# Kernel tuning notes

Hardware: AMD Instinct MI355X
Metric: run time of the kernel (lower is better)

## Reference

```python
import jax, jax.numpy as jnp
from jax import lax
import numpy as np

B, S_DEC, S_ENC = 32, 128, 128
V, E, H = 32000, 200, 128


def setup_inputs() -> dict:
    key = jax.random.key(0)
    ks = jax.random.split(key, 10)
    emb = jax.random.normal(ks[0], (V, E), dtype=jnp.float32)
    emb = emb.at[0].set(0.0)  # padding_idx row (char2id[' '] -> 0)
    return {
        "sequence": jax.random.randint(ks[1], (B, S_DEC), 0, V),
        "hs": jax.random.normal(ks[2], (B, S_ENC, H), dtype=jnp.float32),
        "h": jax.random.normal(ks[3], (1, B, H), dtype=jnp.float32),
        "emb": emb,
        "w_ih": jax.random.normal(ks[4], (3 * H, E), dtype=jnp.float32) * 0.05,
        "w_hh": jax.random.normal(ks[5], (3 * H, H), dtype=jnp.float32) * 0.05,
        "b_ih": jax.random.normal(ks[6], (3 * H,), dtype=jnp.float32) * 0.05,
        "b_hh": jax.random.normal(ks[7], (3 * H,), dtype=jnp.float32) * 0.05,
        "w_out": jax.random.normal(ks[8], (V, 2 * H), dtype=jnp.float32) * 0.05,
        "b_out": jax.random.normal(ks[9], (V,), dtype=jnp.float32) * 0.05,
    }


def _gru(x_gates, h0, w_hh, b_hh):
    # x_gates: [B, S, 3H] precomputed input projections; torch gate order r,z,n
    def step(hprev, xg):
        hg = hprev @ w_hh.T + b_hh
        xr, xz, xn = jnp.split(xg, 3, axis=-1)
        hr, hz, hn = jnp.split(hg, 3, axis=-1)
        r = jax.nn.sigmoid(xr + hr)
        z = jax.nn.sigmoid(xz + hz)
        n = jnp.tanh(xn + r * hn)
        hnew = (1.0 - z) * n + z * hprev
        return hnew, hnew

    hT, outs = lax.scan(step, h0, jnp.swapaxes(x_gates, 0, 1))  # scan over time
    return jnp.swapaxes(outs, 0, 1), hT  # [B,S,H], [B,H]


def reference(sequence, hs, h, emb, w_ih, w_hh, b_ih, b_hh, w_out, b_out):
    # Embedding lookup (padding row already zero)
    x = emb[sequence]  # [B, S_dec, E]
    x_gates = jnp.einsum("bse,ge->bsg", x, w_ih) + b_ih  # [B, S_dec, 3H]
    output, hT = _gru(x_gates, h[0], w_hh, b_hh)  # [B, S_dec, H]
    state = hT[None]  # [1, B, H]
    # s = bmm(hs, output^T): [B, S_enc, S_dec]; softmax over encoder axis (dim=1)
    s = jnp.einsum("beh,bdh->bed", hs, output)
    attention_weight = jax.nn.softmax(s, axis=1)
    # context: replaces the per-timestep python loop with one contraction
    c = jnp.einsum("bed,beh->bdh", attention_weight, hs)  # [B, S_dec, H]
    cat = jnp.concatenate([output, c], axis=-1)  # [B, S_dec, 2H]
    logits = jnp.einsum("bdh,vh->bdv", cat, w_out) + b_out  # [B, S_dec, V]
    return logits, state, attention_weight
```

## Files before the change

kernel.cpp:

```cpp
#include <hip/hip_runtime.h>
#include <hip/hip_bf16.h>

#define B_    32
#define SDEC  128
#define SENC  128
#define V_    32000
#define E_    200
#define H_    128
#define G3    384

typedef __attribute__((ext_vector_type(8))) short bf16x8;
typedef __attribute__((ext_vector_type(4))) float f32x4;

#define GLOBAL_AS __attribute__((address_space(1)))
#define LDS_AS    __attribute__((address_space(3)))

__device__ __forceinline__ float fast_sigmoid(float x) {
  return 1.f / (1.f + __expf(-x));
}
__device__ __forceinline__ float fast_tanh(float x) {
  float e2 = __expf(2.f * x);
  return 1.f - 2.f / (e2 + 1.f);
}

__global__ __launch_bounds__(384) void k_embed_proj(
    const int* __restrict__ seq, const float* __restrict__ emb,
    const float* __restrict__ w_ih, const float* __restrict__ b_ih,
    float* __restrict__ xg) {
  __shared__ __align__(16) float xs[16][E_];
  __shared__ int sidx[16];
  const int r0 = blockIdx.x * 16;
  if (threadIdx.x < 16) sidx[threadIdx.x] = seq[r0 + threadIdx.x];
  __syncthreads();
  for (int i = threadIdx.x; i < 800; i += 384) {
    int r = i / 50, c = i - r * 50;
    *(float4*)&xs[r][c * 4] =
        *(const float4*)(emb + (size_t)sidx[r] * E_ + c * 4);
  }
  __syncthreads();
  const int g = threadIdx.x;
  float acc[16];
#pragma unroll
  for (int r = 0; r < 16; r++) acc[r] = 0.f;
  const float* wg = w_ih + (size_t)g * E_;
  for (int k = 0; k < E_; k += 4) {
    float4 wv = *(const float4*)(wg + k);
#pragma unroll
    for (int r = 0; r < 16; r++) {
      float4 xv = *(const float4*)&xs[r][k];
      acc[r] += wv.x * xv.x + wv.y * xv.y + wv.z * xv.z + wv.w * xv.w;
    }
  }
  const float bb = b_ih[g];
#pragma unroll
  for (int r = 0; r < 16; r++) xg[(size_t)(r0 + r) * G3 + g] = acc[r] + bb;
}

__global__ __launch_bounds__(512) void k_gru_cvt(
    const float* __restrict__ xg, const float* __restrict__ h0,
    const float* __restrict__ w_hh, const float* __restrict__ b_hh,
    float* __restrict__ cat, __hip_bfloat16* __restrict__ cat_bf,
    float* __restrict__ state_out,
    const float* __restrict__ w_out, __hip_bfloat16* __restrict__ wout_bf) {
  if (blockIdx.x >= 32) {
    int idx = ((blockIdx.x - 32) * 512 + threadIdx.x) * 8;
    float4 a = *(const float4*)(w_out + idx);
    float4 c = *(const float4*)(w_out + idx + 4);
    union { __hip_bfloat16 h[8]; uint4 v; } p;
    p.h[0] = __float2bfloat16(a.x); p.h[1] = __float2bfloat16(a.y);
    p.h[2] = __float2bfloat16(a.z); p.h[3] = __float2bfloat16(a.w);
    p.h[4] = __float2bfloat16(c.x); p.h[5] = __float2bfloat16(c.y);
    p.h[6] = __float2bfloat16(c.z); p.h[7] = __float2bfloat16(c.w);
    *(uint4*)(wout_bf + idx) = p.v;
    return;
  }

  const int b = blockIdx.x;
  const int t = threadIdx.x;
  const int hh = t & 127;
  const int q = t >> 7;

  float wr_[32], wz_[32], wn_[32];
#pragma unroll
  for (int j4 = 0; j4 < 8; j4++) {
    *(float4*)&wr_[j4 * 4] =
        *(const float4*)(w_hh + (size_t)hh * H_ + q * 32 + j4 * 4);
    *(float4*)&wz_[j4 * 4] =
        *(const float4*)(w_hh + (size_t)(128 + hh) * H_ + q * 32 + j4 * 4);
    *(float4*)&wn_[j4 * 4] =
        *(const float4*)(w_hh + (size_t)(256 + hh) * H_ + q * 32 + j4 * 4);
  }

  __shared__ __align__(16) float hprev[H_];
  __shared__ float part[3][4][H_];
  float br = 0.f, bz = 0.f, bn = 0.f;
  float cxr = 0.f, cxz = 0.f, cxn = 0.f;
  const float* xgb = xg + (size_t)b * SDEC * G3;
  if (t < H_) {
    hprev[t] = h0[b * H_ + t];
    br = b_hh[hh]; bz = b_hh[128 + hh]; bn = b_hh[256 + hh];
    cxr = xgb[hh]; cxz = xgb[128 + hh]; cxn = xgb[256 + hh];
  }
  float* catb = cat + (size_t)b * SDEC * 256;
  __hip_bfloat16* catbfb = cat_bf + (size_t)b * SDEC * 256;
  __syncthreads();

  for (int s = 0; s < SDEC; s++) {
    float nxr = 0.f, nxz = 0.f, nxn = 0.f;
    if (t < H_ && s + 1 < SDEC) {
      const float* xp = xgb + (size_t)(s + 1) * G3;
      nxr = xp[hh]; nxz = xp[128 + hh]; nxn = xp[256 + hh];
    }
    float sr = 0.f, sz = 0.f, sn = 0.f;
#pragma unroll
    for (int j4 = 0; j4 < 8; j4++) {
      float4 hv = *(const float4*)&hprev[q * 32 + j4 * 4];
      sr += wr_[j4 * 4 + 0] * hv.x + wr_[j4 * 4 + 1] * hv.y +
            wr_[j4 * 4 + 2] * hv.z + wr_[j4 * 4 + 3] * hv.w;
      sz += wz_[j4 * 4 + 0] * hv.x + wz_[j4 * 4 + 1] * hv.y +
            wz_[j4 * 4 + 2] * hv.z + wz_[j4 * 4 + 3] * hv.w;
      sn += wn_[j4 * 4 + 0] * hv.x + wn_[j4 * 4 + 1] * hv.y +
            wn_[j4 * 4 + 2] * hv.z + wn_[j4 * 4 + 3] * hv.w;
    }
    part[0][q][hh] = sr;
    part[1][q][hh] = sz;
    part[2][q][hh] = sn;
    __syncthreads();
    if (t < H_) {
      float hr = part[0][0][hh] + part[0][1][hh] + part[0][2][hh] + part[0][3][hh] + br;
      float hz = part[1][0][hh] + part[1][1][hh] + part[1][2][hh] + part[1][3][hh] + bz;
      float hn = part[2][0][hh] + part[2][1][hh] + part[2][2][hh] + part[2][3][hh] + bn;
      float r = fast_sigmoid(cxr + hr);
      float z = fast_sigmoid(cxz + hz);
      float n = fast_tanh(cxn + r * hn);
      float hnew = (1.f - z) * n + z * hprev[hh];
      hprev[hh] = hnew;
      catb[(size_t)s * 256 + hh] = hnew;
      catbfb[(size_t)s * 256 + hh] = __float2bfloat16(hnew);
    }
    __syncthreads();
    cxr = nxr; cxz = nxz; cxn = nxn;
  }
  if (t < H_) state_out[b * H_ + t] = hprev[t];
}

__global__ __launch_bounds__(256) void k_attn(
    const float* __restrict__ hs, const float* __restrict__ cat,
    float* __restrict__ attw_out, __hip_bfloat16* __restrict__ cat_bf) {
  __shared__ float hsb[SENC][H_ + 1];
  __shared__ float ctb[64][H_ + 1];
  __shared__ float sbuf[SENC][64 + 1];
  const int b = blockIdx.x >> 1;
  const int d0 = (blockIdx.x & 1) * 64;
  const int t = threadIdx.x;
  const float* hsbase = hs + (size_t)b * SENC * H_;

  for (int i = t; i < 4096; i += 256) {
    int r = i >> 5, c = (i & 31) * 4;
    float4 v = *(const float4*)(hsbase + r * H_ + c);
    hsb[r][c] = v.x; hsb[r][c + 1] = v.y; hsb[r][c + 2] = v.z; hsb[r][c + 3] = v.w;
  }
  for (int i = t; i < 2048; i += 256) {
    int r = i >> 5, c = (i & 31) * 4;
    float4 v = *(const float4*)(cat + (size_t)(b * SDEC + d0 + r) * 256 + c);
    ctb[r][c] = v.x; ctb[r][c + 1] = v.y; ctb[r][c + 2] = v.z; ctb[r][c + 3] = v.w;
  }
  __syncthreads();

  {
    const int te = t >> 4, td = t & 15;
    float acc[8][4];
#pragma unroll
    for (int i = 0; i < 8; i++)
#pragma unroll
      for (int j = 0; j < 4; j++) acc[i][j] = 0.f;
#pragma unroll 2
    for (int k = 0; k < H_; k++) {
      float av[8], bv[4];
#pragma unroll
      for (int i = 0; i < 8; i++) av[i] = hsb[te * 8 + i][k];
#pragma unroll
      for (int j = 0; j < 4; j++) bv[j] = ctb[td * 4 + j][k];
#pragma unroll
      for (int i = 0; i < 8; i++)
#pragma unroll
        for (int j = 0; j < 4; j++) acc[i][j] += av[i] * bv[j];
    }
#pragma unroll
    for (int i = 0; i < 8; i++)
#pragma unroll
      for (int j = 0; j < 4; j++) sbuf[te * 8 + i][td * 4 + j] = acc[i][j];
  }
  __syncthreads();

  if (t < 64) {
    const int d = t;
    float m = -1e30f;
    for (int e = 0; e < SENC; e++) m = fmaxf(m, sbuf[e][d]);
    float sum = 0.f;
    for (int e = 0; e < SENC; e++) {
      float p = __expf(sbuf[e][d] - m);
      sbuf[e][d] = p;
      sum += p;
    }
    float inv = 1.f / sum;
    for (int e = 0; e < SENC; e++) {
      float p = sbuf[e][d] * inv;
      sbuf[e][d] = p;
      attw_out[(size_t)b * SENC * SDEC + (size_t)e * SDEC + d0 + d] = p;
    }
  }
  __syncthreads();

  {
    const int td = t >> 4, th = t & 15;
    float acc[4][8];
#pragma unroll
    for (int i = 0; i < 4; i++)
#pragma unroll
      for (int j = 0; j < 8; j++) acc[i][j] = 0.f;
#pragma unroll 2
    for (int e = 0; e < SENC; e++) {
      float pv[4], hv[8];
#pragma unroll
      for (int i = 0; i < 4; i++) pv[i] = sbuf[e][td * 4 + i];
#pragma unroll
      for (int j = 0; j < 8; j++) hv[j] = hsb[e][th + 16 * j];
#pragma unroll
      for (int i = 0; i < 4; i++)
#pragma unroll
        for (int j = 0; j < 8; j++) acc[i][j] += pv[i] * hv[j];
    }
#pragma unroll
    for (int i = 0; i < 4; i++)
#pragma unroll
      for (int j = 0; j < 8; j++)
        cat_bf[(size_t)(b * SDEC + d0 + td * 4 + i) * 256 + 128 + th + 16 * j] =
            __float2bfloat16(acc[i][j]);
  }
}

__global__ __launch_bounds__(512) void k_gemm_mfma(
    const __hip_bfloat16* __restrict__ A, const __hip_bfloat16* __restrict__ Bw,
    const float* __restrict__ b_out, float* __restrict__ C) {
  constexpr int K = 256, N = V_, Kt = 32;
  alignas(16) __shared__ char smem[73728];
  __hip_bfloat16 (*As)[4096] = (__hip_bfloat16(*)[4096])smem;
  __hip_bfloat16 (*Bs)[8192] = (__hip_bfloat16(*)[8192])(smem + 24576);
  float* tr = (float*)smem;

  const int tid = threadIdx.x;
  const int w = tid >> 6, l = tid & 63;
  const int wr = w >> 2, wc = w & 3;
  const int lr = l & 15, lk = l >> 4;
  const int lq = l >> 2, lc = l & 3;

  const int bid = blockIdx.x;
  const int wgid = (bid & 7) * 500 + (bid >> 3);
  const int mt = wgid & 31;
  const int nt = wgid >> 5;
  const int m0 = mt * 128, n0 = nt * 256;

  f32x4 acc[4][4];
#pragma unroll
  for (int m = 0; m < 4; m++)
#pragma unroll
    for (int n = 0; n < 4; n++) acc[m][n] = (f32x4){0.f, 0.f, 0.f, 0.f};

#define STAGE(buf, kk)                                                            \
  do {                                                                            \
    const __hip_bfloat16* gA = A + (size_t)(m0 + w * 16 + lq) * K + (kk) + lc * 8;\
    const __hip_bfloat16* gB0 = Bw + (size_t)(n0 + w * 32 + lq) * K + (kk) + lc * 8;\
    const __hip_bfloat16* gB1 = gB0 + (size_t)16 * K;                             \
    __builtin_amdgcn_global_load_lds((const GLOBAL_AS void*)gA,                   \
        (LDS_AS void*)(&As[buf][w * 512]), 16, 0, 0);                             \
    __builtin_amdgcn_global_load_lds((const GLOBAL_AS void*)gB0,                  \
        (LDS_AS void*)(&Bs[buf][w * 1024]), 16, 0, 0);                            \
    __builtin_amdgcn_global_load_lds((const GLOBAL_AS void*)gB1,                  \
        (LDS_AS void*)(&Bs[buf][w * 1024 + 512]), 16, 0, 0);                      \
  } while (0)

  STAGE(0, 0);
  STAGE(1, Kt);

#pragma unroll
  for (int t = 0; t < 8; ++t) {
    if (t < 7) asm volatile("s_waitcnt vmcnt(3)" ::: "memory");
    else       asm volatile("s_waitcnt vmcnt(0)" ::: "memory");
    __builtin_amdgcn_s_barrier();
    asm volatile("" ::: "memory");

    const int c = t % 3;
    bf16x8 af[4], bfr[4];
#pragma unroll
    for (int m = 0; m < 4; m++)
      af[m] = *(const bf16x8*)(const void*)(&As[c][(wr * 64 + m * 16 + lr) * Kt + lk * 8]);
#pragma unroll
    for (int n = 0; n < 4; n++)
      bfr[n] = *(const bf16x8*)(const void*)(&Bs[c][(wc * 64 + n * 16 + lr) * Kt + lk * 8]);

    if (t < 6) STAGE((t + 2) % 3, (t + 2) * Kt);

#pragma unroll
    for (int m = 0; m < 4; m++)
#pragma unroll
      for (int n = 0; n < 4; n++)
        acc[m][n] = __builtin_amdgcn_mfma_f32_16x16x32_bf16(bfr[n], af[m], acc[m][n], 0, 0, 0);
  }
#undef STAGE

  __syncthreads();
#pragma unroll
  for (int h = 0; h < 2; ++h) {
    if (wr == h) {
#pragma unroll
      for (int m = 0; m < 4; m++) {
#pragma unroll
        for (int n = 0; n < 4; n++) {
          const int row = m * 16 + lr;
          const int col = wc * 64 + n * 16 + lk * 4;
          const float4 bo = *(const float4*)(b_out + n0 + col);
          f32x4 v;
          v[0] = acc[m][n][0] + bo.x;
          v[1] = acc[m][n][1] + bo.y;
          v[2] = acc[m][n][2] + bo.z;
          v[3] = acc[m][n][3] + bo.w;
          *(f32x4*)&tr[row * 260 + col] = v;
        }
      }
    }
    __syncthreads();
#pragma unroll
    for (int i = 0; i < 8; ++i) {
      const int c2 = i * 512 + tid;
      const int row = c2 >> 6;
      const int off = (c2 & 63) * 4;
      f32x4 v = *(const f32x4*)&tr[row * 260 + off];
      __builtin_nontemporal_store(
          v, (f32x4*)(C + (size_t)(m0 + h * 64 + row) * N + n0 + off));
    }
    __syncthreads();
  }
}

extern "C" void kernel_launch(void* const* d_in, const int* in_sizes, int n_in,
                              void* d_out, int out_size, void* d_ws, size_t ws_size,
                              hipStream_t stream) {
  const int* seq = (const int*)d_in[0];
  const float* hs = (const float*)d_in[1];
  const float* h0 = (const float*)d_in[2];
  const float* emb = (const float*)d_in[3];
  const float* w_ih = (const float*)d_in[4];
  const float* w_hh = (const float*)d_in[5];
  const float* b_ih = (const float*)d_in[6];
  const float* b_hh = (const float*)d_in[7];
  const float* w_out = (const float*)d_in[8];
  const float* b_out = (const float*)d_in[9];

  float* out = (float*)d_out;
  float* logits = out;
  float* state = out + 131072000;
  float* attw = out + 131072000 + 4096;

  char* ws = (char*)d_ws;
  float* xg = (float*)ws;
  float* cat = (float*)(ws + 6291456);
  __hip_bfloat16* cat_bf = (__hip_bfloat16*)(ws + 10485760);
  __hip_bfloat16* wout_bf = (__hip_bfloat16*)(ws + 12582912);

  k_embed_proj<<<256, 384, 0, stream>>>(seq, emb, w_ih, b_ih, xg);
  k_gru_cvt<<<2032, 512, 0, stream>>>(xg, h0, w_hh, b_hh, cat, cat_bf, state,
                                      w_out, wout_bf);
  k_attn<<<64, 256, 0, stream>>>(hs, cat, attw, cat_bf);
  k_gemm_mfma<<<4000, 512, 0, stream>>>(cat_bf, wout_bf, b_out, logits);
}
```

Measured before the change: 287.4 us.

## Rework GRU reduction via shuffles, swizzle attention LDS, halve embed-proj threads

The GRU recurrence now gives four adjacent lanes to each hidden unit and reduces their partial dot products with wave shuffles instead of an LDS partial buffer. It double-buffers the hidden state, which removes one barrier per timestep. The attention kernel drops padded LDS arrays in favour of XOR-swizzled float4 layouts, vectorizes the score, softmax and context loops, and writes the bf16 context with packed 16-byte stores. The embedding projection uses 192 threads that each compute two gate rows. The swizzle index arithmetic adds complexity and risks bank conflicts or indexing errors if the permutations are wrong.

```diff
diff --git a/kernel.cpp b/kernel.cpp
--- a/kernel.cpp
+++ b/kernel.cpp
@@ -23,37 +23,44 @@
   return 1.f - 2.f / (e2 + 1.f);
 }
 
-__global__ __launch_bounds__(384) void k_embed_proj(
+__global__ __launch_bounds__(192) void k_embed_proj(
     const int* __restrict__ seq, const float* __restrict__ emb,
     const float* __restrict__ w_ih, const float* __restrict__ b_ih,
     float* __restrict__ xg) {
   __shared__ __align__(16) float xs[16][E_];
   __shared__ int sidx[16];
   const int r0 = blockIdx.x * 16;
-  if (threadIdx.x < 16) sidx[threadIdx.x] = seq[r0 + threadIdx.x];
-  __syncthreads();
-  for (int i = threadIdx.x; i < 800; i += 384) {
+  const int t = threadIdx.x;
+  if (t < 16) sidx[t] = seq[r0 + t];
+  __syncthreads();
+  for (int i = t; i < 800; i += 192) {
     int r = i / 50, c = i - r * 50;
     *(float4*)&xs[r][c * 4] =
         *(const float4*)(emb + (size_t)sidx[r] * E_ + c * 4);
   }
   __syncthreads();
-  const int g = threadIdx.x;
-  float acc[16];
-#pragma unroll
-  for (int r = 0; r < 16; r++) acc[r] = 0.f;
-  const float* wg = w_ih + (size_t)g * E_;
+  const int g0 = t, g1 = t + 192;
+  float a0[16], a1[16];
+#pragma unroll
+  for (int r = 0; r < 16; r++) { a0[r] = 0.f; a1[r] = 0.f; }
+  const float* w0 = w_ih + (size_t)g0 * E_;
+  const float* w1 = w_ih + (size_t)g1 * E_;
   for (int k = 0; k < E_; k += 4) {
-    float4 wv = *(const float4*)(wg + k);
+    float4 wv0 = *(const float4*)(w0 + k);
+    float4 wv1 = *(const float4*)(w1 + k);
 #pragma unroll
     for (int r = 0; r < 16; r++) {
       float4 xv = *(const float4*)&xs[r][k];
-      acc[r] += wv.x * xv.x + wv.y * xv.y + wv.z * xv.z + wv.w * xv.w;
-    }
-  }
-  const float bb = b_ih[g];
-#pragma unroll
-  for (int r = 0; r < 16; r++) xg[(size_t)(r0 + r) * G3 + g] = acc[r] + bb;
+      a0[r] += wv0.x * xv.x + wv0.y * xv.y + wv0.z * xv.z + wv0.w * xv.w;
+      a1[r] += wv1.x * xv.x + wv1.y * xv.y + wv1.z * xv.z + wv1.w * xv.w;
+    }
+  }
+  const float b0 = b_ih[g0], b1 = b_ih[g1];
+#pragma unroll
+  for (int r = 0; r < 16; r++) {
+    xg[(size_t)(r0 + r) * G3 + g0] = a0[r] + b0;
+    xg[(size_t)(r0 + r) * G3 + g1] = a1[r] + b1;
+  }
 }
 
 __global__ __launch_bounds__(512) void k_gru_cvt(
@@ -77,166 +84,195 @@
 
   const int b = blockIdx.x;
   const int t = threadIdx.x;
-  const int hh = t & 127;
-  const int q = t >> 7;
+  const int hh = t >> 2;
+  const int sub = t & 3;
 
   float wr_[32], wz_[32], wn_[32];
 #pragma unroll
-  for (int j4 = 0; j4 < 8; j4++) {
-    *(float4*)&wr_[j4 * 4] =
-        *(const float4*)(w_hh + (size_t)hh * H_ + q * 32 + j4 * 4);
-    *(float4*)&wz_[j4 * 4] =
-        *(const float4*)(w_hh + (size_t)(128 + hh) * H_ + q * 32 + j4 * 4);
-    *(float4*)&wn_[j4 * 4] =
-        *(const float4*)(w_hh + (size_t)(256 + hh) * H_ + q * 32 + j4 * 4);
-  }
-
-  __shared__ __align__(16) float hprev[H_];
-  __shared__ float part[3][4][H_];
-  float br = 0.f, bz = 0.f, bn = 0.f;
-  float cxr = 0.f, cxz = 0.f, cxn = 0.f;
+  for (int m = 0; m < 8; m++) {
+    int c = (m + sub * 2) & 7;
+    int kb = sub * 32 + c * 4;
+    *(float4*)&wr_[m * 4] = *(const float4*)(w_hh + (size_t)hh * H_ + kb);
+    *(float4*)&wz_[m * 4] = *(const float4*)(w_hh + (size_t)(128 + hh) * H_ + kb);
+    *(float4*)&wn_[m * 4] = *(const float4*)(w_hh + (size_t)(256 + hh) * H_ + kb);
+  }
+
+  __shared__ __align__(16) float hp[2][H_];
   const float* xgb = xg + (size_t)b * SDEC * G3;
-  if (t < H_) {
-    hprev[t] = h0[b * H_ + t];
-    br = b_hh[hh]; bz = b_hh[128 + hh]; bn = b_hh[256 + hh];
-    cxr = xgb[hh]; cxz = xgb[128 + hh]; cxn = xgb[256 + hh];
-  }
+  const float br = b_hh[hh], bz = b_hh[128 + hh], bn = b_hh[256 + hh];
+  float cxr = xgb[hh], cxz = xgb[128 + hh], cxn = xgb[256 + hh];
+  if (t < H_) hp[0][t] = h0[b * H_ + t];
   float* catb = cat + (size_t)b * SDEC * 256;
   __hip_bfloat16* catbfb = cat_bf + (size_t)b * SDEC * 256;
   __syncthreads();
 
+  int cur = 0;
   for (int s = 0; s < SDEC; s++) {
     float nxr = 0.f, nxz = 0.f, nxn = 0.f;
-    if (t < H_ && s + 1 < SDEC) {
+    if (s + 1 < SDEC) {
       const float* xp = xgb + (size_t)(s + 1) * G3;
       nxr = xp[hh]; nxz = xp[128 + hh]; nxn = xp[256 + hh];
     }
     float sr = 0.f, sz = 0.f, sn = 0.f;
 #pragma unroll
-    for (int j4 = 0; j4 < 8; j4++) {
-      float4 hv = *(const float4*)&hprev[q * 32 + j4 * 4];
-      sr += wr_[j4 * 4 + 0] * hv.x + wr_[j4 * 4 + 1] * hv.y +
-            wr_[j4 * 4 + 2] * hv.z + wr_[j4 * 4 + 3] * hv.w;
-      sz += wz_[j4 * 4 + 0] * hv.x + wz_[j4 * 4 + 1] * hv.y +
-            wz_[j4 * 4 + 2] * hv.z + wz_[j4 * 4 + 3] * hv.w;
-      sn += wn_[j4 * 4 + 0] * hv.x + wn_[j4 * 4 + 1] * hv.y +
-            wn_[j4 * 4 + 2] * hv.z + wn_[j4 * 4 + 3] * hv.w;
-    }
-    part[0][q][hh] = sr;
-    part[1][q][hh] = sz;
-    part[2][q][hh] = sn;
-    __syncthreads();
-    if (t < H_) {
-      float hr = part[0][0][hh] + part[0][1][hh] + part[0][2][hh] + part[0][3][hh] + br;
-      float hz = part[1][0][hh] + part[1][1][hh] + part[1][2][hh] + part[1][3][hh] + bz;
-      float hn = part[2][0][hh] + part[2][1][hh] + part[2][2][hh] + part[2][3][hh] + bn;
-      float r = fast_sigmoid(cxr + hr);
-      float z = fast_sigmoid(cxz + hz);
-      float n = fast_tanh(cxn + r * hn);
-      float hnew = (1.f - z) * n + z * hprev[hh];
-      hprev[hh] = hnew;
+    for (int m = 0; m < 8; m++) {
+      int c = (m + sub * 2) & 7;
+      float4 hv = *(const float4*)&hp[cur][sub * 32 + c * 4];
+      sr += wr_[m * 4 + 0] * hv.x + wr_[m * 4 + 1] * hv.y +
+            wr_[m * 4 + 2] * hv.z + wr_[m * 4 + 3] * hv.w;
+      sz += wz_[m * 4 + 0] * hv.x + wz_[m * 4 + 1] * hv.y +
+            wz_[m * 4 + 2] * hv.z + wz_[m * 4 + 3] * hv.w;
+      sn += wn_[m * 4 + 0] * hv.x + wn_[m * 4 + 1] * hv.y +
+            wn_[m * 4 + 2] * hv.z + wn_[m * 4 + 3] * hv.w;
+    }
+    sr += __shfl_xor(sr, 1); sr += __shfl_xor(sr, 2);
+    sz += __shfl_xor(sz, 1); sz += __shfl_xor(sz, 2);
+    sn += __shfl_xor(sn, 1); sn += __shfl_xor(sn, 2);
+
+    float hold = hp[cur][hh];
+    float r = fast_sigmoid(cxr + sr + br);
+    float z = fast_sigmoid(cxz + sz + bz);
+    float n = fast_tanh(cxn + r * (sn + bn));
+    float hnew = (1.f - z) * n + z * hold;
+    if (sub == 0) {
+      hp[cur ^ 1][hh] = hnew;
       catb[(size_t)s * 256 + hh] = hnew;
       catbfb[(size_t)s * 256 + hh] = __float2bfloat16(hnew);
     }
     __syncthreads();
+    cur ^= 1;
     cxr = nxr; cxz = nxz; cxn = nxn;
   }
-  if (t < H_) state_out[b * H_ + t] = hprev[t];
+  if (t < H_) state_out[b * H_ + t] = hp[cur][t];
 }
 
 __global__ __launch_bounds__(256) void k_attn(
     const float* __restrict__ hs, const float* __restrict__ cat,
     float* __restrict__ attw_out, __hip_bfloat16* __restrict__ cat_bf) {
-  __shared__ float hsb[SENC][H_ + 1];
-  __shared__ float ctb[64][H_ + 1];
-  __shared__ float sbuf[SENC][64 + 1];
+  __shared__ __align__(16) float hsb[SENC][H_];
+  __shared__ __align__(16) float ctb[64][H_];
+  __shared__ __align__(16) float sbuf[64][SENC];
   const int b = blockIdx.x >> 1;
   const int d0 = (blockIdx.x & 1) * 64;
   const int t = threadIdx.x;
   const float* hsbase = hs + (size_t)b * SENC * H_;
 
   for (int i = t; i < 4096; i += 256) {
-    int r = i >> 5, c = (i & 31) * 4;
-    float4 v = *(const float4*)(hsbase + r * H_ + c);
-    hsb[r][c] = v.x; hsb[r][c + 1] = v.y; hsb[r][c + 2] = v.z; hsb[r][c + 3] = v.w;
+    int r = i >> 5, c4 = i & 31;
+    int pc = c4 ^ ((r >> 3) & 3);
+    *(f32x4*)&hsb[r][pc * 4] = *(const f32x4*)(hsbase + r * H_ + c4 * 4);
   }
   for (int i = t; i < 2048; i += 256) {
-    int r = i >> 5, c = (i & 31) * 4;
-    float4 v = *(const float4*)(cat + (size_t)(b * SDEC + d0 + r) * 256 + c);
-    ctb[r][c] = v.x; ctb[r][c + 1] = v.y; ctb[r][c + 2] = v.z; ctb[r][c + 3] = v.w;
+    int r = i >> 5, c4 = i & 31;
+    int pc = c4 ^ ((r >> 2) & 7);
+    *(f32x4*)&ctb[r][pc * 4] =
+        *(const f32x4*)(cat + (size_t)(b * SDEC + d0 + r) * 256 + c4 * 4);
   }
   __syncthreads();
 
   {
     const int te = t >> 4, td = t & 15;
-    float acc[8][4];
-#pragma unroll
-    for (int i = 0; i < 8; i++)
-#pragma unroll
-      for (int j = 0; j < 4; j++) acc[i][j] = 0.f;
-#pragma unroll 2
-    for (int k = 0; k < H_; k++) {
-      float av[8], bv[4];
-#pragma unroll
-      for (int i = 0; i < 8; i++) av[i] = hsb[te * 8 + i][k];
-#pragma unroll
-      for (int j = 0; j < 4; j++) bv[j] = ctb[td * 4 + j][k];
+    const int sa = te & 3, sb2 = td & 7;
+    float acc[8][4] = {};
+    for (int k4 = 0; k4 < 32; k4++) {
+      const int pa = (k4 ^ sa) * 4, pb = (k4 ^ sb2) * 4;
+      f32x4 av[8], bv[4];
+#pragma unroll
+      for (int i = 0; i < 8; i++) av[i] = *(const f32x4*)&hsb[te * 8 + i][pa];
+#pragma unroll
+      for (int j = 0; j < 4; j++) bv[j] = *(const f32x4*)&ctb[td * 4 + j][pb];
 #pragma unroll
       for (int i = 0; i < 8; i++)
 #pragma unroll
-        for (int j = 0; j < 4; j++) acc[i][j] += av[i] * bv[j];
-    }
-#pragma unroll
-    for (int i = 0; i < 8; i++)
-#pragma unroll
-      for (int j = 0; j < 4; j++) sbuf[te * 8 + i][td * 4 + j] = acc[i][j];
-  }
-  __syncthreads();
-
-  if (t < 64) {
-    const int d = t;
-    float m = -1e30f;
-    for (int e = 0; e < SENC; e++) m = fmaxf(m, sbuf[e][d]);
+        for (int j = 0; j < 4; j++)
+          acc[i][j] += av[i][0] * bv[j][0] + av[i][1] * bv[j][1] +
+                       av[i][2] * bv[j][2] + av[i][3] * bv[j][3];
+    }
+    const int swd = td & 7;
+#pragma unroll
+    for (int j = 0; j < 4; j++) {
+      int drow = td * 4 + j;
+      f32x4 v0 = {acc[0][j], acc[1][j], acc[2][j], acc[3][j]};
+      f32x4 v1 = {acc[4][j], acc[5][j], acc[6][j], acc[7][j]};
+      *(f32x4*)&sbuf[drow][((te * 2) ^ swd) * 4] = v0;
+      *(f32x4*)&sbuf[drow][((te * 2 + 1) ^ swd) * 4] = v1;
+    }
+  }
+  __syncthreads();
+
+  {
+    const int d = t >> 2, p = t & 3;
+    const int swz = (d >> 2) & 7;
+    f32x4 vals[8];
+    float mx = -1e30f;
+#pragma unroll
+    for (int mm = 0; mm < 8; mm++) {
+      int pc = p * 8 + mm;
+      f32x4 v = *(const f32x4*)&sbuf[d][pc * 4];
+      vals[mm] = v;
+      mx = fmaxf(mx, fmaxf(fmaxf(v[0], v[1]), fmaxf(v[2], v[3])));
+    }
+    mx = fmaxf(mx, __shfl_xor(mx, 1));
+    mx = fmaxf(mx, __shfl_xor(mx, 2));
     float sum = 0.f;
-    for (int e = 0; e < SENC; e++) {
-      float p = __expf(sbuf[e][d] - m);
-      sbuf[e][d] = p;
-      sum += p;
-    }
-    float inv = 1.f / sum;
-    for (int e = 0; e < SENC; e++) {
-      float p = sbuf[e][d] * inv;
-      sbuf[e][d] = p;
-      attw_out[(size_t)b * SENC * SDEC + (size_t)e * SDEC + d0 + d] = p;
+#pragma unroll
+    for (int mm = 0; mm < 8; mm++) {
+      f32x4 v = vals[mm];
+      v[0] = __expf(v[0] - mx); v[1] = __expf(v[1] - mx);
+      v[2] = __expf(v[2] - mx); v[3] = __expf(v[3] - mx);
+      vals[mm] = v;
+      sum += v[0] + v[1] + v[2] + v[3];
+    }
+    sum += __shfl_xor(sum, 1); sum += __shfl_xor(sum, 2);
+    const float inv = 1.f / sum;
+    float* aw = attw_out + (size_t)b * SENC * SDEC + d0 + d;
+#pragma unroll
+    for (int mm = 0; mm < 8; mm++) {
+      int pc = p * 8 + mm;
+      f32x4 v = vals[mm];
+      v[0] *= inv; v[1] *= inv; v[2] *= inv; v[3] *= inv;
+      *(f32x4*)&sbuf[d][pc * 4] = v;
+      int c4 = pc ^ swz;
+#pragma unroll
+      for (int u = 0; u < 4; u++)
+        aw[(size_t)(c4 * 4 + u) * SDEC] = v[u];
     }
   }
   __syncthreads();
 
   {
     const int td = t >> 4, th = t & 15;
-    float acc[4][8];
-#pragma unroll
-    for (int i = 0; i < 4; i++)
-#pragma unroll
-      for (int j = 0; j < 8; j++) acc[i][j] = 0.f;
-#pragma unroll 2
-    for (int e = 0; e < SENC; e++) {
-      float pv[4], hv[8];
-#pragma unroll
-      for (int i = 0; i < 4; i++) pv[i] = sbuf[e][td * 4 + i];
-#pragma unroll
-      for (int j = 0; j < 8; j++) hv[j] = hsb[e][th + 16 * j];
-#pragma unroll
-      for (int i = 0; i < 4; i++)
-#pragma unroll
-        for (int j = 0; j < 8; j++) acc[i][j] += pv[i] * hv[j];
-    }
-#pragma unroll
-    for (int i = 0; i < 4; i++)
-#pragma unroll
-      for (int j = 0; j < 8; j++)
-        cat_bf[(size_t)(b * SDEC + d0 + td * 4 + i) * 256 + 128 + th + 16 * j] =
-            __float2bfloat16(acc[i][j]);
+    const int swd = td & 7;
+    float acc[4][8] = {};
+    for (int e4 = 0; e4 < 32; e4++) {
+      const int pp = (e4 ^ swd) * 4;
+      f32x4 pv[4];
+#pragma unroll
+      for (int i = 0; i < 4; i++) pv[i] = *(const f32x4*)&sbuf[td * 4 + i][pp];
+#pragma unroll
+      for (int j = 0; j < 4; j++) {
+        int e = e4 * 4 + j;
+        int sw = (e >> 3) & 3;
+        f32x4 h0v = *(const f32x4*)&hsb[e][((th * 2) ^ sw) * 4];
+        f32x4 h1v = *(const f32x4*)&hsb[e][((th * 2 + 1) ^ sw) * 4];
+#pragma unroll
+        for (int i = 0; i < 4; i++) {
+          float pw = pv[i][j];
+          acc[i][0] += pw * h0v[0]; acc[i][1] += pw * h0v[1];
+          acc[i][2] += pw * h0v[2]; acc[i][3] += pw * h0v[3];
+          acc[i][4] += pw * h1v[0]; acc[i][5] += pw * h1v[1];
+          acc[i][6] += pw * h1v[2]; acc[i][7] += pw * h1v[3];
+        }
+      }
+    }
+#pragma unroll
+    for (int i = 0; i < 4; i++) {
+      union { __hip_bfloat16 hv[8]; uint4 v; } pk;
+#pragma unroll
+      for (int u = 0; u < 8; u++) pk.hv[u] = __float2bfloat16(acc[i][u]);
+      *(uint4*)(cat_bf + (size_t)(b * SDEC + d0 + td * 4 + i) * 256 + 128 +
+                th * 8) = pk.v;
+    }
   }
 }
 
@@ -368,7 +404,7 @@
   __hip_bfloat16* cat_bf = (__hip_bfloat16*)(ws + 10485760);
   __hip_bfloat16* wout_bf = (__hip_bfloat16*)(ws + 12582912);
 
-  k_embed_proj<<<256, 384, 0, stream>>>(seq, emb, w_ih, b_ih, xg);
+  k_embed_proj<<<256, 192, 0, stream>>>(seq, emb, w_ih, b_ih, xg);
   k_gru_cvt<<<2032, 512, 0, stream>>>(xg, h0, w_hh, b_hh, cat, cat_bf, state,
                                       w_out, wout_bf);
   k_attn<<<64, 256, 0, stream>>>(hs, cat, attw, cat_bf);
```

Result: faster. 273.4 us (-4.9%).
